# Optimization experiments

Hardware: AMD Instinct MI355X
Metric: run time of the kernel (lower is better)

Reference implementation:

```python
import jax, jax.numpy as jnp
import numpy as np

B, L, C = 32, 64, 4


def setup_inputs() -> dict:
    key = jax.random.key(0)
    k_idx, k0, k1, k2, k3 = jax.random.split(key, 5)
    # One-hot encoded sequences, flattened to (B, L*C) as the layer expects.
    idx = jax.random.randint(k_idx, (B, L), 0, C)
    x_lc = jax.nn.one_hot(idx, C, dtype=jnp.float32).reshape(B, L * C)
    return {
        "x_lc": x_lc,
        "theta_0": jnp.zeros((1,), dtype=jnp.float32),  # Constant(0.0) init
        "theta_1": 0.05 * jax.random.normal(k1, (L, C), dtype=jnp.float32),
        "theta_2": 0.05 * jax.random.normal(k2, (L, C, L, C), dtype=jnp.float32),
        "theta_3": 0.05 * jax.random.normal(k3, (L, C, L, C, L, C), dtype=jnp.float32),
    }


def reference(x_lc, theta_0, theta_1, theta_2, theta_3):
    Lp, Cp = theta_1.shape
    xr = x_lc.reshape(-1, Lp, Cp)  # (B, L, C)
    pos = jnp.arange(Lp)
    # strict upper-triangular position masks: l0 < l1 (< l2)
    m2 = (pos[None, :] > pos[:, None]).astype(theta_2.dtype)      # (L, L)
    m3 = m2[:, :, None] * m2[None, :, :]                           # (L, L, L)
    # order 1: sum_{l,c} theta_1[l,c] x[b,l,c]
    phi = theta_0[0] + jnp.einsum('ua,bua->b', theta_1, xr)
    # order 2: sum over l0<l1 of theta_2 * x x
    phi = phi + jnp.einsum('uavc,uv,bua,bvc->b', theta_2, m2, xr, xr)
    # order 3: sum over l0<l1<l2 of theta_3 * x x x
    phi = phi + jnp.einsum('uavcwe,uvw,bua,bvc,bwe->b', theta_3, m3, xr, xr, xr)
    return phi.reshape(-1, 1)
```

## Files before the change

kernel.cpp:

```cpp
#include <hip/hip_runtime.h>

#define BB 32
#define LL 64
#define LC 256
#define NPAIR 2016
#define SPS 72
#define WSTRIDE 2048

__global__ __launch_bounds__(256) void pair_kernel(
    const float* __restrict__ x, const float* __restrict__ t2,
    const float* __restrict__ t3, float* __restrict__ ws)
{
    const int t = blockIdx.x;
    const int tid = threadIdx.x;

    int v = (int)((1.0f + sqrtf(8.0f * (float)t + 1.0f)) * 0.5f);
    while (v * (v - 1) / 2 > t) --v;
    while ((v + 1) * v / 2 <= t) ++v;
    const int u = t - v * (v - 1) / 2;

    __shared__ short sp[BB * SPS];
    {
        const float4* __restrict__ x4 = (const float4*)x;
#pragma unroll
        for (int i = 0; i < 8; ++i) {
            int idx = i * 256 + tid;
            float4 f = x4[idx];
            int c = 0; float best = f.x;
            if (f.y > best) { best = f.y; c = 1; }
            if (f.z > best) { best = f.z; c = 2; }
            if (f.w > best) { best = f.w; c = 3; }
            sp[(idx >> 6) * SPS + (idx & 63)] = (short)(((idx & 63) << 2) | c);
        }
    }
    __syncthreads();

    const int b = tid >> 3, k = tid & 7;
    const short* __restrict__ spb = sp + b * SPS;
    const int pu = spb[u], pv = spb[v];
    const float* __restrict__ row = t3 + ((size_t)pu << 16) + ((size_t)pv << 8);

    float acc = 0.0f;
    for (int w = v + 1 + k; w < LL; w += 8)
        acc += row[spb[w]];

    acc += __shfl_down(acc, 4, 8);
    acc += __shfl_down(acc, 2, 8);
    acc += __shfl_down(acc, 1, 8);
    if (k == 0) ws[b * WSTRIDE + t] = acc + t2[pu * LC + pv];
}

__global__ __launch_bounds__(1024) void reduce_kernel(
    const float* __restrict__ x, const float* __restrict__ t0,
    const float* __restrict__ t1, const float* __restrict__ ws,
    float* __restrict__ out)
{
    const int tid = threadIdx.x;
    const int b = tid >> 5, j = tid & 31;
    const float* __restrict__ wsb = ws + b * WSTRIDE;
    float v = 0.0f;
    for (int t = j; t < NPAIR; t += 32) v += wsb[t];

    const float4* __restrict__ x4 = (const float4*)x;
#pragma unroll
    for (int i = 0; i < 2; ++i) {
        int w = j + i * 32;
        float4 f = x4[b * 64 + w];
        int c = 0; float best = f.x;
        if (f.y > best) { best = f.y; c = 1; }
        if (f.z > best) { best = f.z; c = 2; }
        if (f.w > best) { best = f.w; c = 3; }
        v += t1[(w << 2) | c];
    }

    for (int off = 16; off > 0; off >>= 1) v += __shfl_down(v, off, 32);
    if (j == 0) out[b] = v + t0[0];
}

extern "C" void kernel_launch(void* const* d_in, const int* in_sizes, int n_in,
                              void* d_out, int out_size, void* d_ws, size_t ws_size,
                              hipStream_t stream) {
    const float* x  = (const float*)d_in[0];
    const float* t0 = (const float*)d_in[1];
    const float* t1 = (const float*)d_in[2];
    const float* t2 = (const float*)d_in[3];
    const float* t3 = (const float*)d_in[4];
    float* out = (float*)d_out;
    float* ws = (float*)d_ws;

    pair_kernel<<<NPAIR, 256, 0, stream>>>(x, t2, t3, ws);
    reduce_kernel<<<1, 1024, 0, stream>>>(x, t0, t1, ws, out);
}
```

Baseline: 119.5 us.

## Gather theta_3 rows as float4 with register one-hot decode, drop shared staging

The pair kernel no longer decodes the whole one-hot batch into shared memory with a block barrier. Each thread now decodes only the 8 positions it owns into registers and reads theta_3 as aligned float4 vectors, picking the element with selects instead of scattered scalar gathers. The reduce kernel is spread over 32 blocks of 256 threads instead of one 1024-thread block. The float4 loads fetch four times the bytes per needed element, and each thread re-decodes u and v redundantly.

```diff
diff --git a/kernel.cpp b/kernel.cpp
--- a/kernel.cpp
+++ b/kernel.cpp
@@ -4,77 +4,86 @@
 #define LL 64
 #define LC 256
 #define NPAIR 2016
-#define SPS 72
 #define WSTRIDE 2048
 
 __global__ __launch_bounds__(256) void pair_kernel(
     const float* __restrict__ x, const float* __restrict__ t2,
-    const float* __restrict__ t3, float* __restrict__ ws)
+    const float* __restrict__ t3, float* __restrict__ ws2)
 {
     const int t = blockIdx.x;
-    const int tid = threadIdx.x;
-
     int v = (int)((1.0f + sqrtf(8.0f * (float)t + 1.0f)) * 0.5f);
     while (v * (v - 1) / 2 > t) --v;
     while ((v + 1) * v / 2 <= t) ++v;
     const int u = t - v * (v - 1) / 2;
 
-    __shared__ short sp[BB * SPS];
-    {
-        const float4* __restrict__ x4 = (const float4*)x;
+    const int tid = threadIdx.x;
+    const int b = tid >> 3, k = tid & 7;
+    const float4* __restrict__ x4 = (const float4*)x + b * 64;
+
+    int c[8];
 #pragma unroll
-        for (int i = 0; i < 8; ++i) {
-            int idx = i * 256 + tid;
-            float4 f = x4[idx];
-            int c = 0; float best = f.x;
-            if (f.y > best) { best = f.y; c = 1; }
-            if (f.z > best) { best = f.z; c = 2; }
-            if (f.w > best) { best = f.w; c = 3; }
-            sp[(idx >> 6) * SPS + (idx & 63)] = (short)(((idx & 63) << 2) | c);
+    for (int m = 0; m < 8; ++m) {
+        float4 f = x4[8 * m + k];
+        int ci = 0; float best = f.x;
+        if (f.y > best) { best = f.y; ci = 1; }
+        if (f.z > best) { best = f.z; ci = 2; }
+        if (f.w > best) { best = f.w; ci = 3; }
+        c[m] = ci;
+    }
+    float4 fu = x4[u], fv = x4[v];
+    int cu = 0; { float bst = fu.x;
+        if (fu.y > bst) { bst = fu.y; cu = 1; }
+        if (fu.z > bst) { bst = fu.z; cu = 2; }
+        if (fu.w > bst) { bst = fu.w; cu = 3; } }
+    int cv = 0; { float bst = fv.x;
+        if (fv.y > bst) { bst = fv.y; cv = 1; }
+        if (fv.z > bst) { bst = fv.z; cv = 2; }
+        if (fv.w > bst) { bst = fv.w; cv = 3; } }
+    const int pu = 4 * u + cu, pv = 4 * v + cv;
+
+    const float4* __restrict__ row4 =
+        (const float4*)(t3 + ((size_t)pu << 16) + ((size_t)pv << 8));
+
+    float acc = 0.0f;
+    const int mstart = (v + 1 - k + 7) >> 3;
+#pragma unroll
+    for (int m = 0; m < 8; ++m) {
+        if (m >= mstart) {
+            float4 f = row4[8 * m + k];
+            float s0 = (c[m] & 2) ? f.z : f.x;
+            float s1 = (c[m] & 2) ? f.w : f.y;
+            acc += (c[m] & 1) ? s1 : s0;
         }
     }
-    __syncthreads();
-
-    const int b = tid >> 3, k = tid & 7;
-    const short* __restrict__ spb = sp + b * SPS;
-    const int pu = spb[u], pv = spb[v];
-    const float* __restrict__ row = t3 + ((size_t)pu << 16) + ((size_t)pv << 8);
-
-    float acc = 0.0f;
-    for (int w = v + 1 + k; w < LL; w += 8)
-        acc += row[spb[w]];
-
     acc += __shfl_down(acc, 4, 8);
     acc += __shfl_down(acc, 2, 8);
     acc += __shfl_down(acc, 1, 8);
-    if (k == 0) ws[b * WSTRIDE + t] = acc + t2[pu * LC + pv];
+    if (k == 0) ws2[b * WSTRIDE + t] = acc + t2[pu * LC + pv];
 }
 
-__global__ __launch_bounds__(1024) void reduce_kernel(
+__global__ __launch_bounds__(256) void reduce_kernel(
     const float* __restrict__ x, const float* __restrict__ t0,
-    const float* __restrict__ t1, const float* __restrict__ ws,
+    const float* __restrict__ t1, const float* __restrict__ ws2,
     float* __restrict__ out)
 {
+    const int b = blockIdx.x;
     const int tid = threadIdx.x;
-    const int b = tid >> 5, j = tid & 31;
-    const float* __restrict__ wsb = ws + b * WSTRIDE;
+    const float* __restrict__ wsb = ws2 + b * WSTRIDE;
     float v = 0.0f;
-    for (int t = j; t < NPAIR; t += 32) v += wsb[t];
-
-    const float4* __restrict__ x4 = (const float4*)x;
-#pragma unroll
-    for (int i = 0; i < 2; ++i) {
-        int w = j + i * 32;
-        float4 f = x4[b * 64 + w];
+    for (int t = tid; t < NPAIR; t += 256) v += wsb[t];
+    if (tid < LL) {
+        float4 f = ((const float4*)x)[b * 64 + tid];
         int c = 0; float best = f.x;
         if (f.y > best) { best = f.y; c = 1; }
         if (f.z > best) { best = f.z; c = 2; }
         if (f.w > best) { best = f.w; c = 3; }
-        v += t1[(w << 2) | c];
+        v += t1[4 * tid + c];
     }
-
-    for (int off = 16; off > 0; off >>= 1) v += __shfl_down(v, off, 32);
-    if (j == 0) out[b] = v + t0[0];
+    for (int off = 32; off > 0; off >>= 1) v += __shfl_down(v, off, 64);
+    __shared__ float wsum[4];
+    if ((tid & 63) == 0) wsum[tid >> 6] = v;
+    __syncthreads();
+    if (tid == 0) out[b] = wsum[0] + wsum[1] + wsum[2] + wsum[3] + t0[0];
 }
 
 extern "C" void kernel_launch(void* const* d_in, const int* in_sizes, int n_in,
@@ -86,8 +95,8 @@
     const float* t2 = (const float*)d_in[3];
     const float* t3 = (const float*)d_in[4];
     float* out = (float*)d_out;
-    float* ws = (float*)d_ws;
+    float* ws2 = (float*)d_ws;
 
-    pair_kernel<<<NPAIR, 256, 0, stream>>>(x, t2, t3, ws);
-    reduce_kernel<<<1, 1024, 0, stream>>>(x, t0, t1, ws, out);
+    pair_kernel<<<NPAIR, 256, 0, stream>>>(x, t2, t3, ws2);
+    reduce_kernel<<<BB, 256, 0, stream>>>(x, t0, t1, ws2, out);
 }
```

After: 104.7 us. 1.14x faster.
